# Optimization experiments

Measured on AMD Instinct MI355X. Metric: run time of the kernel, lower is better.

Reference implementation:

```python
import jax, jax.numpy as jnp
import numpy as np

B, N = 64, 64
VOCAB, WORD_DIM = 10000, 512
NT, SEM = 30, 16


def _span_indices(n):
    # spans ordered by length k=1..n-1, within each k by left pos l=0..n-k-1
    ls = np.concatenate([np.arange(n - k) for k in range(1, n)])
    rs = np.concatenate([np.arange(n - k) + k for k in range(1, n)])
    return jnp.asarray(ls), jnp.asarray(rs)


def setup_inputs() -> dict:
    key = jax.random.key(0)
    k1, k2, k3, k4 = jax.random.split(key, 4)
    x = jax.random.randint(k1, (B, N), 0, VOCAB)
    lengths = jnp.full((B,), N, dtype=jnp.int64 if jax.config.read('jax_enable_x64') else jnp.int32)
    emb = jax.random.normal(k2, (VOCAB, WORD_DIM), dtype=jnp.float32) * 0.02
    # xavier-uniform for Linear(word_dim -> NT*SEM)
    lim = float(np.sqrt(6.0 / (WORD_DIM + NT * SEM)))
    w_out = jax.random.uniform(k3, (NT * SEM, WORD_DIM), minval=-lim, maxval=lim, dtype=jnp.float32)
    b_out = jnp.zeros((NT * SEM,), dtype=jnp.float32)
    return {"x": x, "lengths": lengths, "emb": emb, "w_out": w_out, "b_out": b_out}


def reference(x, lengths, emb, w_out, b_out):
    b, n = x.shape
    word_emb = emb[x]                                     # [b, N, word_dim]
    h = jnp.einsum('bnd,od->bno', word_emb, w_out) + b_out  # [b, N, NT*SEM]
    mask = (jnp.arange(n)[None, :] < lengths[:, None]).astype(h.dtype)
    wv = (h * mask[:, :, None]).reshape(b, n, NT, SEM)    # [b, N, NT, SEM]
    # prefix sums along sequence -> any contiguous span sum is one subtraction
    prefix = jnp.concatenate([jnp.zeros((b, 1, NT, SEM), h.dtype),
                              jnp.cumsum(wv, axis=1)], axis=1)  # [b, N+1, NT, SEM]
    ls, rs = _span_indices(n)                             # [N(N-1)/2]
    feats = prefix[:, rs + 1] - prefix[:, ls]             # span sums, [b, S, NT, SEM]
    norm = jnp.sqrt(jnp.sum(feats * feats, axis=-1, keepdims=True))
    return feats / norm
```

## Files before the change

### kernel.cpp

```cpp
#include <hip/hip_runtime.h>
#include <hip/hip_bf16.h>
#include <math.h>

#define BB 64
#define NN 64
#define WD 512
#define NTC 30
#define SEMD 16
#define OC 480
#define NSPAN 2016

typedef __bf16 bf16x8 __attribute__((ext_vector_type(8)));
typedef float floatx16 __attribute__((ext_vector_type(16)));

__global__ __launch_bounds__(256) void gemm_prefix_kernel(
    const int* __restrict__ x, const void* __restrict__ emb,
    const void* __restrict__ w, const void* __restrict__ bias,
    float* __restrict__ prefix)
{
    __shared__ float p[2][2][32][32];
    __shared__ float segsum[8][32];
    __shared__ int   sflags[2];

    const int tid  = threadIdx.x;
    const int wv   = tid >> 6;
    const int lane = tid & 63;
    const int b    = blockIdx.y;
    const int o0   = blockIdx.x * 32;

    if (tid < 2) sflags[tid] = 0;
    __syncthreads();
    {
        const __bf16* wb = (const __bf16*)w;
        float v = (float)wb[tid * 2];
        int huge = !(v > -1.0f && v < 1.0f);
        if (huge) atomicOr(&sflags[0], 1);
        if (tid == 0) {
            const int* xi0 = (const int*)x;
            int nz = 0;
            #pragma unroll
            for (int j = 1; j < 16; j += 2) nz |= xi0[j];
            if (nz == 0) sflags[1] = 1;
        }
    }
    __syncthreads();
    const int fp32mode = sflags[0];
    const int x64mode  = sflags[1];

    const int mtile = wv & 1;
    const int kh2   = wv >> 1;
    const int lrow  = lane & 31;
    const int khalf = lane >> 5;
    const int row   = b * 64 + mtile * 32 + lrow;
    const int col   = o0 + lrow;
    const int xi    = x64mode ? x[2 * row] : x[row];
    const int kbase = kh2 * 256 + khalf * 8;

    floatx16 acc = {};
    if (fp32mode) {
        const float* arow = (const float*)emb + (long)xi * WD + kbase;
        const float* brow = (const float*)w   + (long)col * WD + kbase;
        #pragma unroll 4
        for (int k = 0; k < 256; k += 16) {
            float4 a0 = *(const float4*)(arow + k);
            float4 a1 = *(const float4*)(arow + k + 4);
            float4 b0 = *(const float4*)(brow + k);
            float4 b1 = *(const float4*)(brow + k + 4);
            bf16x8 a, bv;
            a[0]=(__bf16)a0.x; a[1]=(__bf16)a0.y; a[2]=(__bf16)a0.z; a[3]=(__bf16)a0.w;
            a[4]=(__bf16)a1.x; a[5]=(__bf16)a1.y; a[6]=(__bf16)a1.z; a[7]=(__bf16)a1.w;
            bv[0]=(__bf16)b0.x; bv[1]=(__bf16)b0.y; bv[2]=(__bf16)b0.z; bv[3]=(__bf16)b0.w;
            bv[4]=(__bf16)b1.x; bv[5]=(__bf16)b1.y; bv[6]=(__bf16)b1.z; bv[7]=(__bf16)b1.w;
            acc = __builtin_amdgcn_mfma_f32_32x32x16_bf16(a, bv, acc, 0, 0, 0);
        }
    } else {
        const __bf16* arow = (const __bf16*)emb + (long)xi * WD + kbase;
        const __bf16* brow = (const __bf16*)w   + (long)col * WD + kbase;
        #pragma unroll 8
        for (int k = 0; k < 256; k += 16) {
            bf16x8 a = *(const bf16x8*)(arow + k);
            bf16x8 bv = *(const bf16x8*)(brow + k);
            acc = __builtin_amdgcn_mfma_f32_32x32x16_bf16(a, bv, acc, 0, 0, 0);
        }
    }

    #pragma unroll
    for (int r = 0; r < 16; ++r) {
        const int m = (r & 3) + 8 * (r >> 2) + 4 * khalf;
        p[mtile][kh2][m][lrow] = acc[r];
    }
    __syncthreads();

    const int o   = tid & 31;
    const int seg = tid >> 5;
    const float bo = fp32mode ? ((const float*)bias)[o0 + o]
                              : (float)((const __bf16*)bias)[o0 + o];
    float vals[8];
    float run = 0.f;
    #pragma unroll
    for (int j = 0; j < 8; ++j) {
        const int n  = seg * 8 + j;
        const int mt = n >> 5, mm = n & 31;
        float v = p[mt][0][mm][o] + p[mt][1][mm][o] + bo;
        vals[j] = v;
        run += v;
    }
    segsum[seg][o] = run;
    __syncthreads();

    float base = 0.f;
    #pragma unroll
    for (int j = 0; j < 7; ++j)
        if (j < seg) base += segsum[j][o];

    float* pref = prefix + ((long)b * 65) * OC + o0 + o;
    if (seg == 0) pref[0] = 0.f;
    float acc2 = base;
    #pragma unroll
    for (int j = 0; j < 8; ++j) {
        acc2 += vals[j];
        const int n = seg * 8 + j;
        pref[(long)(n + 1) * OC] = acc2;
    }
}

__global__ __launch_bounds__(256) void span_kernel(
    const float* __restrict__ prefix, float* __restrict__ out)
{
    const int g   = blockIdx.x * 256 + threadIdx.x;
    const int q   = g & 3;
    const int idx = g >> 2;
    const int nt  = idx % NTC;
    const int t   = idx / NTC;
    const int s   = t % NSPAN;
    const int b   = t / NSPAN;

    int k = (int)((127.0f - sqrtf(16129.0f - 8.0f * (float)s)) * 0.5f) + 1;
    while (64 * k - ((k * (k + 1)) >> 1) <= s) ++k;
    while (64 * (k - 1) - (((k - 1) * k) >> 1) > s) --k;
    const int fkm1 = 64 * (k - 1) - (((k - 1) * k) >> 1);
    const int l = s - fkm1;
    const int r = l + k + 1;

    const long rowbase = ((long)b * 65) * OC + nt * SEMD + q * 4;
    const float4 a = *(const float4*)(prefix + rowbase + (long)l * OC);
    const float4 c = *(const float4*)(prefix + rowbase + (long)r * OC);

    float4 d;
    d.x = c.x - a.x; d.y = c.y - a.y; d.z = c.z - a.z; d.w = c.w - a.w;
    float ss = d.x * d.x + d.y * d.y + d.z * d.z + d.w * d.w;
    ss += __shfl_xor(ss, 1);
    ss += __shfl_xor(ss, 2);
    const float inv = rsqrtf(fmaxf(ss, 1e-30f));

    float4 v;
    v.x = d.x * inv; v.y = d.y * inv; v.z = d.z * inv; v.w = d.w * inv;
    *(float4*)(out + (long)g * 4) = v;
}

extern "C" void kernel_launch(void* const* d_in, const int* in_sizes, int n_in,
                              void* d_out, int out_size, void* d_ws, size_t ws_size,
                              hipStream_t stream) {
    const int*  x    = (const int*)d_in[0];
    const void* emb  = d_in[2];
    const void* w    = d_in[3];
    const void* bias = d_in[4];
    float*      out  = (float*)d_out;

    float* prefix = (float*)d_ws;

    gemm_prefix_kernel<<<dim3(15, BB), 256, 0, stream>>>(x, emb, w, bias, prefix);

    const int total4 = BB * NSPAN * NTC * 4;
    span_kernel<<<total4 / 256, 256, 0, stream>>>(prefix, out);
}
```

Baseline: 298.0 us.

## Loop span kernel over NT per thread with nontemporal output stores

The span kernel is restructured so that each 4-thread group owns one span and loops over all 30 NT slices, using a 2D grid (span block, batch). This removes the per-thread div/mod index decoding and the k-solving sqrt from the inner work, since both are now done once per span rather than once per (span, NT). Output is written with nontemporal stores to avoid polluting the cache with the large write stream. The change cuts thread-level parallelism per block (128 threads) and makes each group of four lanes write a strided 64-byte chunk per iteration, which may reduce store coalescing per instruction.

```diff
diff --git a/kernel.cpp b/kernel.cpp
--- a/kernel.cpp
+++ b/kernel.cpp
@@ -12,6 +12,7 @@
 
 typedef __bf16 bf16x8 __attribute__((ext_vector_type(8)));
 typedef float floatx16 __attribute__((ext_vector_type(16)));
+typedef float floatx4 __attribute__((ext_vector_type(4)));
 
 __global__ __launch_bounds__(256) void gemm_prefix_kernel(
     const int* __restrict__ x, const void* __restrict__ emb,
@@ -124,16 +125,13 @@
     }
 }
 
-__global__ __launch_bounds__(256) void span_kernel(
+__global__ __launch_bounds__(128) void span_kernel(
     const float* __restrict__ prefix, float* __restrict__ out)
 {
-    const int g   = blockIdx.x * 256 + threadIdx.x;
-    const int q   = g & 3;
-    const int idx = g >> 2;
-    const int nt  = idx % NTC;
-    const int t   = idx / NTC;
-    const int s   = t % NSPAN;
-    const int b   = t / NSPAN;
+    const int tid = threadIdx.x;
+    const int q   = tid & 3;
+    const int s   = blockIdx.x * 32 + (tid >> 2);
+    const int b   = blockIdx.y;
 
     int k = (int)((127.0f - sqrtf(16129.0f - 8.0f * (float)s)) * 0.5f) + 1;
     while (64 * k - ((k * (k + 1)) >> 1) <= s) ++k;
@@ -142,20 +140,24 @@
     const int l = s - fkm1;
     const int r = l + k + 1;
 
-    const long rowbase = ((long)b * 65) * OC + nt * SEMD + q * 4;
-    const float4 a = *(const float4*)(prefix + rowbase + (long)l * OC);
-    const float4 c = *(const float4*)(prefix + rowbase + (long)r * OC);
+    const float* pl = prefix + ((long)b * 65 + l) * OC + q * 4;
+    const float* pr = prefix + ((long)b * 65 + r) * OC + q * 4;
+    float* op = out + ((long)(b * NSPAN + s) * NTC) * SEMD + q * 4;
 
-    float4 d;
-    d.x = c.x - a.x; d.y = c.y - a.y; d.z = c.z - a.z; d.w = c.w - a.w;
-    float ss = d.x * d.x + d.y * d.y + d.z * d.z + d.w * d.w;
-    ss += __shfl_xor(ss, 1);
-    ss += __shfl_xor(ss, 2);
-    const float inv = rsqrtf(fmaxf(ss, 1e-30f));
-
-    float4 v;
-    v.x = d.x * inv; v.y = d.y * inv; v.z = d.z * inv; v.w = d.w * inv;
-    *(float4*)(out + (long)g * 4) = v;
+    #pragma unroll 6
+    for (int nt = 0; nt < NTC; ++nt) {
+        const float4 a = *(const float4*)(pl + nt * SEMD);
+        const float4 c = *(const float4*)(pr + nt * SEMD);
+        float4 d;
+        d.x = c.x - a.x; d.y = c.y - a.y; d.z = c.z - a.z; d.w = c.w - a.w;
+        float ss = d.x * d.x + d.y * d.y + d.z * d.z + d.w * d.w;
+        ss += __shfl_xor(ss, 1);
+        ss += __shfl_xor(ss, 2);
+        const float inv = rsqrtf(fmaxf(ss, 1e-30f));
+        floatx4 v;
+        v[0] = d.x * inv; v[1] = d.y * inv; v[2] = d.z * inv; v[3] = d.w * inv;
+        __builtin_nontemporal_store(v, (floatx4*)(op + nt * SEMD));
+    }
 }
 
 extern "C" void kernel_launch(void* const* d_in, const int* in_sizes, int n_in,
@@ -171,6 +173,5 @@
 
     gemm_prefix_kernel<<<dim3(15, BB), 256, 0, stream>>>(x, emb, w, bias, prefix);
 
-    const int total4 = BB * NSPAN * NTC * 4;
-    span_kernel<<<total4 / 256, 256, 0, stream>>>(prefix, out);
+    span_kernel<<<dim3(63, BB), 128, 0, stream>>>(prefix, out);
 }
```

Result: slower. 315.3 us (+5.8%).
